# Optimization experiments

Measured on AMD Instinct MI355X. Metric: run time of the kernel, lower is better.

Reference implementation:

```python
import jax, jax.numpy as jnp
import numpy as np

RESERVOIR_DIM = 2048
INPUT_DIM = 1024
LEAK_RATE = 0.1
SPIKE_THRESHOLD = 0.5
MAX_RESERVOIR_DIM = 4096
BATCH = 4096


def setup_inputs() -> dict:
    key = jax.random.key(0)
    k1, k2, k3, k4, k5 = jax.random.split(key, 5)
    inputs = jax.random.normal(k1, (BATCH, 1, INPUT_DIM), dtype=jnp.float32)
    state = jax.random.normal(k2, (BATCH, 1, MAX_RESERVOIR_DIM), dtype=jnp.float32)
    # glorot-ish scaled weights
    reservoir_weights = jax.random.normal(k3, (MAX_RESERVOIR_DIM, MAX_RESERVOIR_DIM), dtype=jnp.float32) * (1.0 / np.sqrt(MAX_RESERVOIR_DIM))
    input_weights = jax.random.normal(k4, (MAX_RESERVOIR_DIM, INPUT_DIM), dtype=jnp.float32) * (1.0 / np.sqrt(INPUT_DIM))
    gate_weights = jax.random.normal(k5, (3 * MAX_RESERVOIR_DIM, INPUT_DIM), dtype=jnp.float32) * (1.0 / np.sqrt(INPUT_DIM))
    return {"inputs": inputs, "state": state, "reservoir_weights": reservoir_weights,
            "input_weights": input_weights, "gate_weights": gate_weights}


def reference(inputs, state, reservoir_weights, input_weights, gate_weights):
    R = RESERVOIR_DIM
    x = jnp.squeeze(inputs, axis=1)                      # [B, D]
    prev_state = jnp.squeeze(state, axis=1)[:, :R]       # [B, R]
    # three small matmuls on sliced weights
    input_part = x @ input_weights[:R, :].T              # [B, R]
    reservoir_part = prev_state @ reservoir_weights[:R, :R]  # [B, R]
    gate_part = x @ gate_weights[:3 * R, :].T            # [B, 3R]
    i_gate, f_gate, o_gate = jnp.split(jax.nn.sigmoid(gate_part), 3, axis=-1)
    new_state = (1.0 - LEAK_RATE) * (f_gate * prev_state) + LEAK_RATE * jnp.tanh(i_gate * (input_part + reservoir_part))
    new_state = o_gate * new_state
    # spike threshold: subtract threshold where state exceeds it
    new_state = jnp.where(new_state > SPIKE_THRESHOLD, new_state - SPIKE_THRESHOLD, new_state)
    padded = jnp.pad(new_state, ((0, 0), (0, MAX_RESERVOIR_DIM - R)))  # [B, max]
    padded = padded[:, None, :]                          # [B, 1, max]
    return padded
```

## Files before the change

### kernel.cpp

```cpp
#include <hip/hip_runtime.h>
#include <math.h>

constexpr int M    = 4096;
constexpr int K1   = 1024;
constexpr int R    = 2048;
constexpr int MAXR = 4096;

constexpr int BM = 128;
constexpr int BN = 32;
constexpr int BK = 32;
constexpr int BKP = BK + 8;

typedef _Float16 f16x8 __attribute__((ext_vector_type(8)));
typedef _Float16 f16x4 __attribute__((ext_vector_type(4)));
typedef float    f32x4 __attribute__((ext_vector_type(4)));

__device__ __forceinline__ void split4(const float4 v, f16x4* hi, f16x4* lo) {
    float a[4] = {v.x, v.y, v.z, v.w};
    f16x4 h, l;
#pragma unroll
    for (int j = 0; j < 4; ++j) {
        _Float16 hh = (_Float16)a[j];
        h[j] = hh;
        l[j] = (_Float16)((a[j] - (float)hh) * 1024.0f);
    }
    *hi = h; *lo = l;
}

__global__ __launch_bounds__(256, 2)
void slnn_mfma_kernel(const float* __restrict__ X,
                      const float* __restrict__ S,
                      const float* __restrict__ Wres,
                      const float* __restrict__ Win,
                      const float* __restrict__ Wg,
                      float* __restrict__ out)
{
    __shared__ _Float16 Ah[BM][BKP];
    __shared__ _Float16 Al[BM][BKP];
    __shared__ _Float16 Bh[4][BN][BKP];
    __shared__ _Float16 Bl[4][BN][BKP];

    const int tid  = threadIdx.x;
    const int w    = tid >> 6;
    const int lane = tid & 63;
    const int row0 = blockIdx.x * BM;
    const int col0 = blockIdx.y * BN;

    const int lrow = lane & 15;
    const int koff = (lane >> 4) * 8;

    const int s_r  = tid >> 3;
    const int s_kq = tid & 7;

    f32x4 hh[4][2][2] = {};
    f32x4 cx[4][2][2] = {};

    for (int k0 = 0; k0 < K1; k0 += BK) {
#pragma unroll
        for (int i = 0; i < 4; ++i) {
            const int row = s_r + 32 * i;
            float4 v = *(const float4*)(X + (size_t)(row0 + row) * K1 + k0 + s_kq * 4);
            f16x4 h, l; split4(v, &h, &l);
            *(f16x4*)&Ah[row][s_kq * 4] = h;
            *(f16x4*)&Al[row][s_kq * 4] = l;
        }
        {
            const int n = s_r;
            f16x4 h, l;
            float4 v0 = *(const float4*)(Win + (size_t)(col0 + n) * K1 + k0 + s_kq * 4);
            split4(v0, &h, &l);
            *(f16x4*)&Bh[0][n][s_kq * 4] = h;
            *(f16x4*)&Bl[0][n][s_kq * 4] = l;
#pragma unroll
            for (int g = 1; g < 4; ++g) {
                float4 v = *(const float4*)(Wg + (size_t)(col0 + n + (g - 1) * R) * K1 + k0 + s_kq * 4);
                split4(v, &h, &l);
                *(f16x4*)&Bh[g][n][s_kq * 4] = h;
                *(f16x4*)&Bl[g][n][s_kq * 4] = l;
            }
        }
        __syncthreads();

        f16x8 ah[2], al[2];
#pragma unroll
        for (int mf = 0; mf < 2; ++mf) {
            const int m = w * 32 + mf * 16 + lrow;
            ah[mf] = *(const f16x8*)&Ah[m][koff];
            al[mf] = *(const f16x8*)&Al[m][koff];
        }
#pragma unroll
        for (int g = 0; g < 4; ++g) {
#pragma unroll
            for (int nf = 0; nf < 2; ++nf) {
                const int n = nf * 16 + lrow;
                f16x8 bh = *(const f16x8*)&Bh[g][n][koff];
                f16x8 bl = *(const f16x8*)&Bl[g][n][koff];
#pragma unroll
                for (int mf = 0; mf < 2; ++mf) {
                    hh[g][mf][nf] = __builtin_amdgcn_mfma_f32_16x16x32_f16(ah[mf], bh, hh[g][mf][nf], 0, 0, 0);
                    cx[g][mf][nf] = __builtin_amdgcn_mfma_f32_16x16x32_f16(ah[mf], bl, cx[g][mf][nf], 0, 0, 0);
                    cx[g][mf][nf] = __builtin_amdgcn_mfma_f32_16x16x32_f16(al[mf], bh, cx[g][mf][nf], 0, 0, 0);
                }
            }
        }
        __syncthreads();
    }

#pragma unroll
    for (int g = 0; g < 4; ++g)
#pragma unroll
        for (int mf = 0; mf < 2; ++mf)
#pragma unroll
            for (int nf = 0; nf < 2; ++nf)
                hh[g][mf][nf] += cx[g][mf][nf] * (1.0f / 1024.0f);

    f32x4 rhh[2][2] = {};
    f32x4 rcx[2][2] = {};
    const int wn  = tid & 31;
    const int wkb = (tid >> 5) * 4;

    for (int k0 = 0; k0 < R; k0 += BK) {
#pragma unroll
        for (int i = 0; i < 4; ++i) {
            const int row = s_r + 32 * i;
            float4 v = *(const float4*)(S + (size_t)(row0 + row) * MAXR + k0 + s_kq * 4);
            f16x4 h, l; split4(v, &h, &l);
            *(f16x4*)&Ah[row][s_kq * 4] = h;
            *(f16x4*)&Al[row][s_kq * 4] = l;
        }
        {
            float4 v;
            v.x = Wres[(size_t)(k0 + wkb + 0) * MAXR + col0 + wn];
            v.y = Wres[(size_t)(k0 + wkb + 1) * MAXR + col0 + wn];
            v.z = Wres[(size_t)(k0 + wkb + 2) * MAXR + col0 + wn];
            v.w = Wres[(size_t)(k0 + wkb + 3) * MAXR + col0 + wn];
            f16x4 h, l; split4(v, &h, &l);
            *(f16x4*)&Bh[0][wn][wkb] = h;
            *(f16x4*)&Bl[0][wn][wkb] = l;
        }
        __syncthreads();

        f16x8 ah[2], al[2];
#pragma unroll
        for (int mf = 0; mf < 2; ++mf) {
            const int m = w * 32 + mf * 16 + lrow;
            ah[mf] = *(const f16x8*)&Ah[m][koff];
            al[mf] = *(const f16x8*)&Al[m][koff];
        }
#pragma unroll
        for (int nf = 0; nf < 2; ++nf) {
            const int n = nf * 16 + lrow;
            f16x8 bh = *(const f16x8*)&Bh[0][n][koff];
            f16x8 bl = *(const f16x8*)&Bl[0][n][koff];
#pragma unroll
            for (int mf = 0; mf < 2; ++mf) {
                rhh[mf][nf] = __builtin_amdgcn_mfma_f32_16x16x32_f16(ah[mf], bh, rhh[mf][nf], 0, 0, 0);
                rcx[mf][nf] = __builtin_amdgcn_mfma_f32_16x16x32_f16(ah[mf], bl, rcx[mf][nf], 0, 0, 0);
                rcx[mf][nf] = __builtin_amdgcn_mfma_f32_16x16x32_f16(al[mf], bh, rcx[mf][nf], 0, 0, 0);
            }
        }
        __syncthreads();
    }
#pragma unroll
    for (int mf = 0; mf < 2; ++mf)
#pragma unroll
        for (int nf = 0; nf < 2; ++nf)
            rhh[mf][nf] += rcx[mf][nf] * (1.0f / 1024.0f);

#pragma unroll
    for (int mf = 0; mf < 2; ++mf) {
#pragma unroll
        for (int nf = 0; nf < 2; ++nf) {
#pragma unroll
            for (int i = 0; i < 4; ++i) {
                const int row = row0 + w * 32 + mf * 16 + (lane >> 4) * 4 + i;
                const int col = col0 + nf * 16 + (lane & 15);
                const float p   = S[(size_t)row * MAXR + col];
                const float vin = hh[0][mf][nf][i];
                const float vi  = hh[1][mf][nf][i];
                const float vf  = hh[2][mf][nf][i];
                const float vo  = hh[3][mf][nf][i];
                const float vr  = rhh[mf][nf][i];
                const float ig = 1.0f / (1.0f + expf(-vi));
                const float fg = 1.0f / (1.0f + expf(-vf));
                const float og = 1.0f / (1.0f + expf(-vo));
                float s = 0.9f * (fg * p) + 0.1f * tanhf(ig * (vin + vr));
                s *= og;
                if (s > 0.5f) s -= 0.5f;
                out[(size_t)row * MAXR + col] = s;
                out[(size_t)row * MAXR + R + col] = 0.0f;
            }
        }
    }
}

extern "C" void kernel_launch(void* const* d_in, const int* in_sizes, int n_in,
                              void* d_out, int out_size, void* d_ws, size_t ws_size,
                              hipStream_t stream) {
    const float* X    = (const float*)d_in[0];
    const float* S    = (const float*)d_in[1];
    const float* Wres = (const float*)d_in[2];
    const float* Win  = (const float*)d_in[3];
    const float* Wg   = (const float*)d_in[4];
    float* out = (float*)d_out;

    dim3 grid(M / BM, R / BN);
    slnn_mfma_kernel<<<grid, dim3(256), 0, stream>>>(X, S, Wres, Win, Wg, out);
}
```

Measured before the change: 684.4 us.

## Pre-split operands to fp16 hi/lo in workspace and stream via global_load_lds

Adds conversion kernels that split X, S, the gate/input weights and the reservoir weights into fp16 hi/lo arrays in a k-chunked layout stored in workspace. The main GEMM kernel then loads these tiles straight into LDS with global_load_lds instead of converting fp32 to split fp16 in every block. This removes the repeated split work and the strided Wres reads from the inner loop. In exchange it adds extra launches and a full pass over the weights and activations every call, and it only takes this path when the workspace is large enough.

Result: faster. 555.4 us (-18.8%).

```diff
diff --git a/kernel.cpp b/kernel.cpp
--- a/kernel.cpp
+++ b/kernel.cpp
@@ -15,6 +15,17 @@
 typedef _Float16 f16x4 __attribute__((ext_vector_type(4)));
 typedef float    f32x4 __attribute__((ext_vector_type(4)));
 
+constexpr size_t WS_XH = 0;
+constexpr size_t WS_XL = 8388608;
+constexpr size_t WS_SH = 16777216;
+constexpr size_t WS_SL = 33554432;
+constexpr size_t WS_GH = 50331648;
+constexpr size_t WS_GL = 67108864;
+constexpr size_t WS_RH = 83886080;
+constexpr size_t WS_RL = 92274688;
+constexpr size_t WS_NEED = 100663296;
+constexpr size_t G_MAT_HALFS = 2097152;
+
 __device__ __forceinline__ void split4(const float4 v, f16x4* hi, f16x4* lo) {
     float a[4] = {v.x, v.y, v.z, v.w};
     f16x4 h, l;
@@ -27,18 +38,80 @@
     *hi = h; *lo = l;
 }
 
+__device__ __forceinline__ void glds16(const void* g, void* l) {
+    __builtin_amdgcn_global_load_lds((const __attribute__((address_space(1))) void*)g,
+                                     (__attribute__((address_space(3))) void*)l, 16, 0, 0);
+}
+
+__global__ __launch_bounds__(256)
+void convert_rowmajor(const float* __restrict__ in, int in_stride,
+                      _Float16* __restrict__ outH, _Float16* __restrict__ outL, int nrows)
+{
+    __shared__ _Float16 lh[64][136];
+    __shared__ _Float16 ll[64][136];
+    const int t  = threadIdx.x;
+    const int r0 = blockIdx.x * 64;
+    const int k0 = blockIdx.y * 128;
+#pragma unroll
+    for (int i = 0; i < 8; ++i) {
+        int idx = i * 256 + t; int kq = idx & 31; int r = idx >> 5;
+        float4 v = *(const float4*)(in + (size_t)(r0 + r) * in_stride + k0 + kq * 4);
+        f16x4 h, l; split4(v, &h, &l);
+        *(f16x4*)&lh[r][kq * 4] = h;
+        *(f16x4*)&ll[r][kq * 4] = l;
+    }
+    __syncthreads();
+#pragma unroll
+    for (int i = 0; i < 4; ++i) {
+        int idx = i * 256 + t; int r = idx & 63; int c = idx >> 6;
+        size_t o = ((size_t)(k0 >> 3) + c) * nrows + r0 + r;
+        *((f16x8*)outH + o) = *(const f16x8*)&lh[r][c * 8];
+        *((f16x8*)outL + o) = *(const f16x8*)&ll[r][c * 8];
+    }
+}
+
+__global__ __launch_bounds__(256)
+void convert_colmajor(const float* __restrict__ in, int in_stride,
+                      _Float16* __restrict__ outH, _Float16* __restrict__ outL, int ncols)
+{
+    __shared__ _Float16 lh[64][136];
+    __shared__ _Float16 ll[64][136];
+    const int t  = threadIdx.x;
+    const int k0 = blockIdx.x * 128;
+    const int n0 = blockIdx.y * 64;
+#pragma unroll
+    for (int i = 0; i < 8; ++i) {
+        int idx = i * 256 + t; int n4 = idx & 15; int k = idx >> 4;
+        float4 v = *(const float4*)(in + (size_t)(k0 + k) * in_stride + n0 + n4 * 4);
+        float a[4] = {v.x, v.y, v.z, v.w};
+#pragma unroll
+        for (int j = 0; j < 4; ++j) {
+            _Float16 h = (_Float16)a[j];
+            lh[n4 * 4 + j][k] = h;
+            ll[n4 * 4 + j][k] = (_Float16)((a[j] - (float)h) * 1024.0f);
+        }
+    }
+    __syncthreads();
+#pragma unroll
+    for (int i = 0; i < 4; ++i) {
+        int idx = i * 256 + t; int r = idx & 63; int c = idx >> 6;
+        size_t o = ((size_t)(k0 >> 3) + c) * ncols + n0 + r;
+        *((f16x8*)outH + o) = *(const f16x8*)&lh[r][c * 8];
+        *((f16x8*)outL + o) = *(const f16x8*)&ll[r][c * 8];
+    }
+}
+
 __global__ __launch_bounds__(256, 2)
-void slnn_mfma_kernel(const float* __restrict__ X,
-                      const float* __restrict__ S,
-                      const float* __restrict__ Wres,
-                      const float* __restrict__ Win,
-                      const float* __restrict__ Wg,
-                      float* __restrict__ out)
+void slnn_mfma_pre(const _Float16* __restrict__ XH, const _Float16* __restrict__ XL,
+                   const _Float16* __restrict__ SH, const _Float16* __restrict__ SL,
+                   const _Float16* __restrict__ GH, const _Float16* __restrict__ GL,
+                   const _Float16* __restrict__ RH, const _Float16* __restrict__ RL,
+                   const float* __restrict__ S, float* __restrict__ out)
 {
-    __shared__ _Float16 Ah[BM][BKP];
-    __shared__ _Float16 Al[BM][BKP];
-    __shared__ _Float16 Bh[4][BN][BKP];
-    __shared__ _Float16 Bl[4][BN][BKP];
+    __shared__ _Float16 AH[4096];
+    __shared__ _Float16 AL[4096];
+    __shared__ _Float16 BH[4096];
+    __shared__ _Float16 BL[4096];
 
     const int tid  = threadIdx.x;
     const int w    = tid >> 6;
@@ -46,55 +119,39 @@
     const int row0 = blockIdx.x * BM;
     const int col0 = blockIdx.y * BN;
 
-    const int lrow = lane & 15;
-    const int koff = (lane >> 4) * 8;
-
-    const int s_r  = tid >> 3;
-    const int s_kq = tid & 7;
+    const int lr = lane & 15;
+    const int sl = lane >> 4;
 
     f32x4 hh[4][2][2] = {};
     f32x4 cx[4][2][2] = {};
 
-    for (int k0 = 0; k0 < K1; k0 += BK) {
-#pragma unroll
-        for (int i = 0; i < 4; ++i) {
-            const int row = s_r + 32 * i;
-            float4 v = *(const float4*)(X + (size_t)(row0 + row) * K1 + k0 + s_kq * 4);
-            f16x4 h, l; split4(v, &h, &l);
-            *(f16x4*)&Ah[row][s_kq * 4] = h;
-            *(f16x4*)&Al[row][s_kq * 4] = l;
-        }
-        {
-            const int n = s_r;
-            f16x4 h, l;
-            float4 v0 = *(const float4*)(Win + (size_t)(col0 + n) * K1 + k0 + s_kq * 4);
-            split4(v0, &h, &l);
-            *(f16x4*)&Bh[0][n][s_kq * 4] = h;
-            *(f16x4*)&Bl[0][n][s_kq * 4] = l;
-#pragma unroll
-            for (int g = 1; g < 4; ++g) {
-                float4 v = *(const float4*)(Wg + (size_t)(col0 + n + (g - 1) * R) * K1 + k0 + s_kq * 4);
-                split4(v, &h, &l);
-                *(f16x4*)&Bh[g][n][s_kq * 4] = h;
-                *(f16x4*)&Bl[g][n][s_kq * 4] = l;
-            }
+    for (int kt = 0; kt < 32; ++kt) {
+#pragma unroll
+        for (int p = 0; p < 2; ++p) {
+            size_t ga = ((size_t)(kt * 4 + w)) * 4096 + row0 + p * 64 + lane;
+            glds16(XH + ga * 8, &AH[(w * 128 + p * 64) * 8]);
+            glds16(XL + ga * 8, &AL[(w * 128 + p * 64) * 8]);
+            int slot = 2 * p + (lane >> 5);
+            size_t gb = (size_t)w * G_MAT_HALFS / 8 + ((size_t)(kt * 4 + slot)) * 2048 + col0 + (lane & 31);
+            glds16(GH + gb * 8, &BH[(w * 128 + p * 64) * 8]);
+            glds16(GL + gb * 8, &BL[(w * 128 + p * 64) * 8]);
         }
         __syncthreads();
 
         f16x8 ah[2], al[2];
 #pragma unroll
         for (int mf = 0; mf < 2; ++mf) {
-            const int m = w * 32 + mf * 16 + lrow;
-            ah[mf] = *(const f16x8*)&Ah[m][koff];
-            al[mf] = *(const f16x8*)&Al[m][koff];
+            const int ch = sl * 128 + w * 32 + mf * 16 + lr;
+            ah[mf] = *(const f16x8*)&AH[ch * 8];
+            al[mf] = *(const f16x8*)&AL[ch * 8];
         }
 #pragma unroll
         for (int g = 0; g < 4; ++g) {
 #pragma unroll
             for (int nf = 0; nf < 2; ++nf) {
-                const int n = nf * 16 + lrow;
-                f16x8 bh = *(const f16x8*)&Bh[g][n][koff];
-                f16x8 bl = *(const f16x8*)&Bl[g][n][koff];
+                const int ch = g * 128 + sl * 32 + nf * 16 + lr;
+                f16x8 bh = *(const f16x8*)&BH[ch * 8];
+                f16x8 bl = *(const f16x8*)&BL[ch * 8];
 #pragma unroll
                 for (int mf = 0; mf < 2; ++mf) {
                     hh[g][mf][nf] = __builtin_amdgcn_mfma_f32_16x16x32_f16(ah[mf], bh, hh[g][mf][nf], 0, 0, 0);
@@ -116,42 +173,35 @@
 
     f32x4 rhh[2][2] = {};
     f32x4 rcx[2][2] = {};
-    const int wn  = tid & 31;
-    const int wkb = (tid >> 5) * 4;
-
-    for (int k0 = 0; k0 < R; k0 += BK) {
-#pragma unroll
-        for (int i = 0; i < 4; ++i) {
-            const int row = s_r + 32 * i;
-            float4 v = *(const float4*)(S + (size_t)(row0 + row) * MAXR + k0 + s_kq * 4);
-            f16x4 h, l; split4(v, &h, &l);
-            *(f16x4*)&Ah[row][s_kq * 4] = h;
-            *(f16x4*)&Al[row][s_kq * 4] = l;
+    for (int kt = 0; kt < 64; ++kt) {
+#pragma unroll
+        for (int p = 0; p < 2; ++p) {
+            size_t ga = ((size_t)(kt * 4 + w)) * 4096 + row0 + p * 64 + lane;
+            glds16(SH + ga * 8, &AH[(w * 128 + p * 64) * 8]);
+            glds16(SL + ga * 8, &AL[(w * 128 + p * 64) * 8]);
         }
         {
-            float4 v;
-            v.x = Wres[(size_t)(k0 + wkb + 0) * MAXR + col0 + wn];
-            v.y = Wres[(size_t)(k0 + wkb + 1) * MAXR + col0 + wn];
-            v.z = Wres[(size_t)(k0 + wkb + 2) * MAXR + col0 + wn];
-            v.w = Wres[(size_t)(k0 + wkb + 3) * MAXR + col0 + wn];
-            f16x4 h, l; split4(v, &h, &l);
-            *(f16x4*)&Bh[0][wn][wkb] = h;
-            *(f16x4*)&Bl[0][wn][wkb] = l;
+            const int j = w & 1;
+            const _Float16* src = (w < 2) ? RH : RL;
+            _Float16* dst = (w < 2) ? BH : BL;
+            const int slot = 2 * j + (lane >> 5);
+            size_t gb = ((size_t)(kt * 4 + slot)) * 2048 + col0 + (lane & 31);
+            glds16(src + gb * 8, &dst[(j * 64) * 8]);
         }
         __syncthreads();
 
         f16x8 ah[2], al[2];
 #pragma unroll
         for (int mf = 0; mf < 2; ++mf) {
-            const int m = w * 32 + mf * 16 + lrow;
-            ah[mf] = *(const f16x8*)&Ah[m][koff];
-            al[mf] = *(const f16x8*)&Al[m][koff];
+            const int ch = sl * 128 + w * 32 + mf * 16 + lr;
+            ah[mf] = *(const f16x8*)&AH[ch * 8];
+            al[mf] = *(const f16x8*)&AL[ch * 8];
         }
 #pragma unroll
         for (int nf = 0; nf < 2; ++nf) {
-            const int n = nf * 16 + lrow;
-            f16x8 bh = *(const f16x8*)&Bh[0][n][koff];
-            f16x8 bl = *(const f16x8*)&Bl[0][n][koff];
+            const int ch = sl * 32 + nf * 16 + lr;
+            f16x8 bh = *(const f16x8*)&BH[ch * 8];
+            f16x8 bl = *(const f16x8*)&BL[ch * 8];
 #pragma unroll
             for (int mf = 0; mf < 2; ++mf) {
                 rhh[mf][nf] = __builtin_amdgcn_mfma_f32_16x16x32_f16(ah[mf], bh, rhh[mf][nf], 0, 0, 0);
@@ -194,6 +244,164 @@
     }
 }
 
+__global__ __launch_bounds__(256, 2)
+void slnn_mfma_kernel(const float* __restrict__ X, const float* __restrict__ S,
+                      const float* __restrict__ Wres, const float* __restrict__ Win,
+                      const float* __restrict__ Wg, float* __restrict__ out)
+{
+    __shared__ _Float16 Ah[BM][BKP];
+    __shared__ _Float16 Al[BM][BKP];
+    __shared__ _Float16 Bh[4][BN][BKP];
+    __shared__ _Float16 Bl[4][BN][BKP];
+
+    const int tid  = threadIdx.x;
+    const int w    = tid >> 6;
+    const int lane = tid & 63;
+    const int row0 = blockIdx.x * BM;
+    const int col0 = blockIdx.y * BN;
+    const int lrow = lane & 15;
+    const int koff = (lane >> 4) * 8;
+    const int s_r  = tid >> 3;
+    const int s_kq = tid & 7;
+
+    f32x4 hh[4][2][2] = {};
+    f32x4 cx[4][2][2] = {};
+
+    for (int k0 = 0; k0 < K1; k0 += BK) {
+#pragma unroll
+        for (int i = 0; i < 4; ++i) {
+            const int row = s_r + 32 * i;
+            float4 v = *(const float4*)(X + (size_t)(row0 + row) * K1 + k0 + s_kq * 4);
+            f16x4 h, l; split4(v, &h, &l);
+            *(f16x4*)&Ah[row][s_kq * 4] = h;
+            *(f16x4*)&Al[row][s_kq * 4] = l;
+        }
+        {
+            const int n = s_r;
+            f16x4 h, l;
+            float4 v0 = *(const float4*)(Win + (size_t)(col0 + n) * K1 + k0 + s_kq * 4);
+            split4(v0, &h, &l);
+            *(f16x4*)&Bh[0][n][s_kq * 4] = h;
+            *(f16x4*)&Bl[0][n][s_kq * 4] = l;
+#pragma unroll
+            for (int g = 1; g < 4; ++g) {
+                float4 v = *(const float4*)(Wg + (size_t)(col0 + n + (g - 1) * R) * K1 + k0 + s_kq * 4);
+                split4(v, &h, &l);
+                *(f16x4*)&Bh[g][n][s_kq * 4] = h;
+                *(f16x4*)&Bl[g][n][s_kq * 4] = l;
+            }
+        }
+        __syncthreads();
+        f16x8 ah[2], al[2];
+#pragma unroll
+        for (int mf = 0; mf < 2; ++mf) {
+            const int m = w * 32 + mf * 16 + lrow;
+            ah[mf] = *(const f16x8*)&Ah[m][koff];
+            al[mf] = *(const f16x8*)&Al[m][koff];
+        }
+#pragma unroll
+        for (int g = 0; g < 4; ++g) {
+#pragma unroll
+            for (int nf = 0; nf < 2; ++nf) {
+                const int n = nf * 16 + lrow;
+                f16x8 bh = *(const f16x8*)&Bh[g][n][koff];
+                f16x8 bl = *(const f16x8*)&Bl[g][n][koff];
+#pragma unroll
+                for (int mf = 0; mf < 2; ++mf) {
+                    hh[g][mf][nf] = __builtin_amdgcn_mfma_f32_16x16x32_f16(ah[mf], bh, hh[g][mf][nf], 0, 0, 0);
+                    cx[g][mf][nf] = __builtin_amdgcn_mfma_f32_16x16x32_f16(ah[mf], bl, cx[g][mf][nf], 0, 0, 0);
+                    cx[g][mf][nf] = __builtin_amdgcn_mfma_f32_16x16x32_f16(al[mf], bh, cx[g][mf][nf], 0, 0, 0);
+                }
+            }
+        }
+        __syncthreads();
+    }
+#pragma unroll
+    for (int g = 0; g < 4; ++g)
+#pragma unroll
+        for (int mf = 0; mf < 2; ++mf)
+#pragma unroll
+            for (int nf = 0; nf < 2; ++nf)
+                hh[g][mf][nf] += cx[g][mf][nf] * (1.0f / 1024.0f);
+
+    f32x4 rhh[2][2] = {};
+    f32x4 rcx[2][2] = {};
+    const int wn  = tid & 31;
+    const int wkb = (tid >> 5) * 4;
+    for (int k0 = 0; k0 < R; k0 += BK) {
+#pragma unroll
+        for (int i = 0; i < 4; ++i) {
+            const int row = s_r + 32 * i;
+            float4 v = *(const float4*)(S + (size_t)(row0 + row) * MAXR + k0 + s_kq * 4);
+            f16x4 h, l; split4(v, &h, &l);
+            *(f16x4*)&Ah[row][s_kq * 4] = h;
+            *(f16x4*)&Al[row][s_kq * 4] = l;
+        }
+        {
+            float4 v;
+            v.x = Wres[(size_t)(k0 + wkb + 0) * MAXR + col0 + wn];
+            v.y = Wres[(size_t)(k0 + wkb + 1) * MAXR + col0 + wn];
+            v.z = Wres[(size_t)(k0 + wkb + 2) * MAXR + col0 + wn];
+            v.w = Wres[(size_t)(k0 + wkb + 3) * MAXR + col0 + wn];
+            f16x4 h, l; split4(v, &h, &l);
+            *(f16x4*)&Bh[0][wn][wkb] = h;
+            *(f16x4*)&Bl[0][wn][wkb] = l;
+        }
+        __syncthreads();
+        f16x8 ah[2], al[2];
+#pragma unroll
+        for (int mf = 0; mf < 2; ++mf) {
+            const int m = w * 32 + mf * 16 + lrow;
+            ah[mf] = *(const f16x8*)&Ah[m][koff];
+            al[mf] = *(const f16x8*)&Al[m][koff];
+        }
+#pragma unroll
+        for (int nf = 0; nf < 2; ++nf) {
+            const int n = nf * 16 + lrow;
+            f16x8 bh = *(const f16x8*)&Bh[0][n][koff];
+            f16x8 bl = *(const f16x8*)&Bl[0][n][koff];
+#pragma unroll
+            for (int mf = 0; mf < 2; ++mf) {
+                rhh[mf][nf] = __builtin_amdgcn_mfma_f32_16x16x32_f16(ah[mf], bh, rhh[mf][nf], 0, 0, 0);
+                rcx[mf][nf] = __builtin_amdgcn_mfma_f32_16x16x32_f16(ah[mf], bl, rcx[mf][nf], 0, 0, 0);
+                rcx[mf][nf] = __builtin_amdgcn_mfma_f32_16x16x32_f16(al[mf], bh, rcx[mf][nf], 0, 0, 0);
+            }
+        }
+        __syncthreads();
+    }
+#pragma unroll
+    for (int mf = 0; mf < 2; ++mf)
+#pragma unroll
+        for (int nf = 0; nf < 2; ++nf)
+            rhh[mf][nf] += rcx[mf][nf] * (1.0f / 1024.0f);
+
+#pragma unroll
+    for (int mf = 0; mf < 2; ++mf) {
+#pragma unroll
+        for (int nf = 0; nf < 2; ++nf) {
+#pragma unroll
+            for (int i = 0; i < 4; ++i) {
+                const int row = row0 + w * 32 + mf * 16 + (lane >> 4) * 4 + i;
+                const int col = col0 + nf * 16 + (lane & 15);
+                const float p   = S[(size_t)row * MAXR + col];
+                const float vin = hh[0][mf][nf][i];
+                const float vi  = hh[1][mf][nf][i];
+                const float vf  = hh[2][mf][nf][i];
+                const float vo  = hh[3][mf][nf][i];
+                const float vr  = rhh[mf][nf][i];
+                const float ig = 1.0f / (1.0f + expf(-vi));
+                const float fg = 1.0f / (1.0f + expf(-vf));
+                const float og = 1.0f / (1.0f + expf(-vo));
+                float s = 0.9f * (fg * p) + 0.1f * tanhf(ig * (vin + vr));
+                s *= og;
+                if (s > 0.5f) s -= 0.5f;
+                out[(size_t)row * MAXR + col] = s;
+                out[(size_t)row * MAXR + R + col] = 0.0f;
+            }
+        }
+    }
+}
+
 extern "C" void kernel_launch(void* const* d_in, const int* in_sizes, int n_in,
                               void* d_out, int out_size, void* d_ws, size_t ws_size,
                               hipStream_t stream) {
@@ -203,7 +411,31 @@
     const float* Win  = (const float*)d_in[3];
     const float* Wg   = (const float*)d_in[4];
     float* out = (float*)d_out;
-
     dim3 grid(M / BM, R / BN);
-    slnn_mfma_kernel<<<grid, dim3(256), 0, stream>>>(X, S, Wres, Win, Wg, out);
-}
+
+    if (ws_size >= WS_NEED) {
+        char* ws = (char*)d_ws;
+        _Float16* XH = (_Float16*)(ws + WS_XH);
+        _Float16* XL = (_Float16*)(ws + WS_XL);
+        _Float16* SHp = (_Float16*)(ws + WS_SH);
+        _Float16* SLp = (_Float16*)(ws + WS_SL);
+        _Float16* GHp = (_Float16*)(ws + WS_GH);
+        _Float16* GLp = (_Float16*)(ws + WS_GL);
+        _Float16* RHp = (_Float16*)(ws + WS_RH);
+        _Float16* RLp = (_Float16*)(ws + WS_RL);
+
+        convert_rowmajor<<<dim3(64, 8),  256, 0, stream>>>(X, K1, XH, XL, 4096);
+        convert_rowmajor<<<dim3(64, 16), 256, 0, stream>>>(S, MAXR, SHp, SLp, 4096);
+        convert_rowmajor<<<dim3(32, 8),  256, 0, stream>>>(Win, K1, GHp, GLp, 2048);
+        for (int g = 0; g < 3; ++g) {
+            convert_rowmajor<<<dim3(32, 8), 256, 0, stream>>>(
+                Wg + (size_t)g * 2048 * K1, K1,
+                GHp + (size_t)(g + 1) * G_MAT_HALFS, GLp + (size_t)(g + 1) * G_MAT_HALFS, 2048);
+        }
+        convert_colmajor<<<dim3(16, 32), 256, 0, stream>>>(Wres, MAXR, RHp, RLp, 2048);
+
+        slnn_mfma_pre<<<grid, dim3(256), 0, stream>>>(XH, XL, SHp, SLp, GHp, GLp, RHp, RLp, S, out);
+    } else {
+        slnn_mfma_kernel<<<grid, dim3(256), 0, stream>>>(X, S, Wres, Win, Wg, out);
+    }
+}
```
